# Kernel tuning notes

Measured on AMD Instinct MI355X. Metric: run time of the kernel, lower is better.

Reference implementation:

```python
import jax, jax.numpy as jnp
import numpy as np
import math

HIDDEN = 2048
N_HEADS = 16
HEAD_DIM = HIDDEN // N_HEADS
ROPE_BASE = 10000.0


def setup_inputs() -> dict:
    key = jax.random.key(0)
    ks = jax.random.split(key, 5)
    B, S = 2, 2048
    hidden_states = jax.random.normal(ks[0], (B, S, HIDDEN), dtype=jnp.float32)
    # additive causal mask (bsz, 1, q_len, kv_len)
    causal = jnp.tril(jnp.ones((S, S), dtype=bool))
    attention_mask = jnp.where(causal, 0.0, jnp.finfo(jnp.float32).min)[None, None].astype(jnp.float32)
    attention_mask = jnp.broadcast_to(attention_mask, (B, 1, S, S))
    position_ids = jnp.broadcast_to(jnp.arange(S, dtype=jnp.int32)[None], (B, S))
    scale = 1.0 / math.sqrt(HIDDEN)
    Wq = jax.random.normal(ks[1], (HIDDEN, HIDDEN), dtype=jnp.float32) * scale
    Wk = jax.random.normal(ks[2], (HIDDEN, HIDDEN), dtype=jnp.float32) * scale
    Wv = jax.random.normal(ks[3], (HIDDEN, HIDDEN), dtype=jnp.float32) * scale
    Wo = jax.random.normal(ks[4], (HIDDEN, HIDDEN), dtype=jnp.float32) * scale
    return {"hidden_states": hidden_states, "attention_mask": attention_mask,
            "position_ids": position_ids, "Wq": Wq, "Wk": Wk, "Wv": Wv, "Wo": Wo}


def _rotate_half(x):
    x1, x2 = jnp.split(x, 2, axis=-1)
    return jnp.concatenate([-x2, x1], axis=-1)


def _rope_cos_sin(position_ids, head_dim, dtype):
    inv_freq = 1.0 / (ROPE_BASE ** (jnp.arange(0, head_dim, 2, dtype=jnp.float32) / head_dim))
    freqs = position_ids.astype(jnp.float32)[..., None] * inv_freq  # [B, S, hd/2]
    emb = jnp.concatenate([freqs, freqs], axis=-1)                  # [B, S, hd]
    # unsqueeze head dim -> [B, 1, S, hd]
    return jnp.cos(emb)[:, None].astype(dtype), jnp.sin(emb)[:, None].astype(dtype)


def reference(hidden_states, attention_mask, position_ids, Wq, Wk, Wv, Wo):
    B, S, _ = hidden_states.shape
    H, D = N_HEADS, HEAD_DIM
    # projections (nn.Linear: x @ W.T); split heads -> [B, H, S, D]
    def proj(W):
        return jnp.einsum('bsh,oh->bso', hidden_states, W).reshape(B, S, H, D).transpose(0, 2, 1, 3)
    q, k, v = proj(Wq), proj(Wk), proj(Wv)
    cos, sin = _rope_cos_sin(position_ids, D, hidden_states.dtype)
    q = q * cos + _rotate_half(q) * sin
    k = k * cos + _rotate_half(k) * sin
    scores = jnp.einsum('bhqd,bhkd->bhqk', q, k) / math.sqrt(D)
    scores = scores + attention_mask
    probs = jax.nn.softmax(scores.astype(jnp.float32), axis=-1).astype(q.dtype)
    attn = jnp.einsum('bhqk,bhkd->bhqd', probs, v)
    attn = attn.transpose(0, 2, 1, 3).reshape(B, S, H * D)
    return jnp.einsum('bso,ho->bsh', attn, Wo)
```

## Files before the change

kernel.cpp:

```cpp
#include <hip/hip_runtime.h>
#include <cstdint>

typedef unsigned short u16t;
typedef float v4f __attribute__((ext_vector_type(4)));
typedef short v8s __attribute__((ext_vector_type(8)));

#define HIDDEN 2048
#define NHEAD 16
#define HDIM 128
#define SEQ 2048
#define BATCH 2
#define MROWS (BATCH * SEQ)

__device__ __forceinline__ float bf2f(u16t u) {
  return __builtin_bit_cast(float, (uint32_t)((uint32_t)u << 16));
}
__device__ __forceinline__ u16t f2bf(float f) {
  uint32_t u = __builtin_bit_cast(uint32_t, f);
  u += 0x7FFFu + ((u >> 16) & 1u);
  return (u16t)(u >> 16);
}
__device__ __forceinline__ ushort4 f2bf4(float4 v) {
  ushort4 r;
  r.x = f2bf(v.x); r.y = f2bf(v.y); r.z = f2bf(v.z); r.w = f2bf(v.w);
  return r;
}

__device__ __forceinline__ void gld_lds16(const u16t* g, u16t* l) {
  __builtin_amdgcn_global_load_lds(
      (const __attribute__((address_space(1))) uint32_t*)g,
      (__attribute__((address_space(3))) uint32_t*)l, 16, 0, 0);
}

__global__ __launch_bounds__(256) void cvt_bf16(const float* __restrict__ src,
                                                u16t* __restrict__ dst, int n8) {
  int i = blockIdx.x * 256 + threadIdx.x;
  if (i < n8) {
    float4 a = ((const float4*)src)[2 * i];
    float4 b = ((const float4*)src)[2 * i + 1];
    union { ushort4 h[2]; uint4 u; } pk;
    pk.h[0] = f2bf4(a);
    pk.h[1] = f2bf4(b);
    ((uint4*)dst)[i] = pk.u;
  }
}

__global__ __launch_bounds__(256) void cvt_bf16_w4(
    const float* __restrict__ s0, const float* __restrict__ s1,
    const float* __restrict__ s2, const float* __restrict__ s3,
    u16t* __restrict__ d0, u16t* __restrict__ d1,
    u16t* __restrict__ d2, u16t* __restrict__ d3) {
  int i = blockIdx.x * 256 + threadIdx.x;
  int sel = i >> 19;
  int j = i & 0x7FFFF;
  const float* src = (sel == 0) ? s0 : (sel == 1) ? s1 : (sel == 2) ? s2 : s3;
  u16t* dst = (sel == 0) ? d0 : (sel == 1) ? d1 : (sel == 2) ? d2 : d3;
  float4 a = ((const float4*)src)[2 * j];
  float4 b = ((const float4*)src)[2 * j + 1];
  union { ushort4 h[2]; uint4 u; } pk;
  pk.h[0] = f2bf4(a);
  pk.h[1] = f2bf4(b);
  ((uint4*)dst)[j] = pk.u;
}

template <int B_BF16, int OUT_F32>
__global__ __launch_bounds__(256) void gemm_a16(const u16t* __restrict__ A,
                                                const void* __restrict__ Bp,
                                                void* __restrict__ Cp) {
  __shared__ u16t As[128 * 32];
  __shared__ u16t Bs[128 * 32];

  const int n0 = blockIdx.x * 128;
  const int m0 = blockIdx.y * 128;
  const int t = threadIdx.x;
  const int lane = t & 63;
  const int w = t >> 6;
  const int wm = w & 1;
  const int wn = w >> 1;
  const int l15 = lane & 15;
  const int quad = lane >> 4;

  v4f acc[4][4];
#pragma unroll
  for (int i = 0; i < 4; ++i)
#pragma unroll
    for (int j = 0; j < 4; ++j) acc[i][j] = (v4f){0.f, 0.f, 0.f, 0.f};

  for (int kb = 0; kb < HIDDEN; kb += 32) {
#pragma unroll
    for (int j = 0; j < 2; ++j) {
      int idx = t + j * 256;
      int row = idx >> 2;
      int ch = (idx & 3) * 8;
      gld_lds16(&A[(size_t)(m0 + row) * HIDDEN + kb + ch], &As[idx * 8]);
      if (B_BF16)
        gld_lds16(&((const u16t*)Bp)[(size_t)(n0 + row) * HIDDEN + kb + ch], &Bs[idx * 8]);
    }
    if (!B_BF16) {
      const float* B = (const float*)Bp;
#pragma unroll
      for (int j = 0; j < 4; ++j) {
        int idx = t + j * 256;
        int row = idx >> 3;
        int c4 = (idx & 7) * 4;
        float4 bv = *(const float4*)&B[(size_t)(n0 + row) * HIDDEN + kb + c4];
        *(ushort4*)&Bs[row * 32 + c4] = f2bf4(bv);
      }
    }
    __syncthreads();

    v8s af[4], bf[4];
#pragma unroll
    for (int mt = 0; mt < 4; ++mt)
      af[mt] = *(const v8s*)&As[(wm * 64 + mt * 16 + l15) * 32 + quad * 8];
#pragma unroll
    for (int nt = 0; nt < 4; ++nt)
      bf[nt] = *(const v8s*)&Bs[(wn * 64 + nt * 16 + l15) * 32 + quad * 8];

#pragma unroll
    for (int mt = 0; mt < 4; ++mt)
#pragma unroll
      for (int nt = 0; nt < 4; ++nt)
        acc[mt][nt] = __builtin_amdgcn_mfma_f32_16x16x32_bf16(af[mt], bf[nt], acc[mt][nt], 0, 0, 0);
    __syncthreads();
  }

#pragma unroll
  for (int mt = 0; mt < 4; ++mt) {
#pragma unroll
    for (int nt = 0; nt < 4; ++nt) {
      int col = n0 + wn * 64 + nt * 16 + l15;
#pragma unroll
      for (int r = 0; r < 4; ++r) {
        int row = m0 + wm * 64 + mt * 16 + quad * 4 + r;
        if (OUT_F32)
          ((float*)Cp)[(size_t)row * HIDDEN + col] = acc[mt][nt][r];
        else
          ((u16t*)Cp)[(size_t)row * HIDDEN + col] = f2bf(acc[mt][nt][r]);
      }
    }
  }
}

template <int B_BF16>
__global__ __launch_bounds__(256) void gemm_vt(const u16t* __restrict__ A,
                                               const void* __restrict__ Bp,
                                               u16t* __restrict__ VtOut) {
  __shared__ u16t As[128 * 32];
  __shared__ u16t Bs[128 * 32];
  __shared__ u16t Ct[128 * 136];

  const int n0 = blockIdx.x * 128;
  const int m0 = blockIdx.y * 128;
  const int t = threadIdx.x;
  const int lane = t & 63;
  const int w = t >> 6;
  const int wm = w & 1;
  const int wn = w >> 1;
  const int l15 = lane & 15;
  const int quad = lane >> 4;

  v4f acc[4][4];
#pragma unroll
  for (int i = 0; i < 4; ++i)
#pragma unroll
    for (int j = 0; j < 4; ++j) acc[i][j] = (v4f){0.f, 0.f, 0.f, 0.f};

  for (int kb = 0; kb < HIDDEN; kb += 32) {
#pragma unroll
    for (int j = 0; j < 2; ++j) {
      int idx = t + j * 256;
      int row = idx >> 2;
      int ch = (idx & 3) * 8;
      gld_lds16(&A[(size_t)(m0 + row) * HIDDEN + kb + ch], &As[idx * 8]);
      if (B_BF16)
        gld_lds16(&((const u16t*)Bp)[(size_t)(n0 + row) * HIDDEN + kb + ch], &Bs[idx * 8]);
    }
    if (!B_BF16) {
      const float* B = (const float*)Bp;
#pragma unroll
      for (int j = 0; j < 4; ++j) {
        int idx = t + j * 256;
        int row = idx >> 3;
        int c4 = (idx & 7) * 4;
        float4 bv = *(const float4*)&B[(size_t)(n0 + row) * HIDDEN + kb + c4];
        *(ushort4*)&Bs[row * 32 + c4] = f2bf4(bv);
      }
    }
    __syncthreads();

    v8s af[4], bf[4];
#pragma unroll
    for (int mt = 0; mt < 4; ++mt)
      af[mt] = *(const v8s*)&As[(wm * 64 + mt * 16 + l15) * 32 + quad * 8];
#pragma unroll
    for (int nt = 0; nt < 4; ++nt)
      bf[nt] = *(const v8s*)&Bs[(wn * 64 + nt * 16 + l15) * 32 + quad * 8];

#pragma unroll
    for (int mt = 0; mt < 4; ++mt)
#pragma unroll
      for (int nt = 0; nt < 4; ++nt)
        acc[mt][nt] = __builtin_amdgcn_mfma_f32_16x16x32_bf16(af[mt], bf[nt], acc[mt][nt], 0, 0, 0);
    __syncthreads();
  }

#pragma unroll
  for (int mt = 0; mt < 4; ++mt)
#pragma unroll
    for (int nt = 0; nt < 4; ++nt)
#pragma unroll
      for (int r = 0; r < 4; ++r)
        Ct[(wn * 64 + nt * 16 + l15) * 136 + (wm * 64 + mt * 16 + quad * 4 + r)] =
            f2bf(acc[mt][nt][r]);
  __syncthreads();

#pragma unroll
  for (int j = 0; j < 8; ++j) {
    int idx = t + j * 256;
    int nl = idx >> 4;
    int mc = idx & 15;
    *(uint4*)&VtOut[(size_t)(n0 + nl) * MROWS + m0 + mc * 8] =
        *(const uint4*)&Ct[nl * 136 + mc * 8];
  }
}

__global__ __launch_bounds__(256) void rope_k(u16t* __restrict__ q, u16t* __restrict__ k) {
  int idx = blockIdx.x * 256 + threadIdx.x;
  int i = idx & 63;
  int h = (idx >> 6) & (NHEAD - 1);
  int m = idx >> 10;
  int s = m & (SEQ - 1);
  float inv = __expf(-(float)i * 0.14391156831212787f);
  float th = (float)s * inv;
  float sn, cs;
  __sincosf(th, &sn, &cs);
  size_t base = (size_t)m * HIDDEN + h * HDIM + i;
  {
    float a = bf2f(q[base]), b = bf2f(q[base + 64]);
    q[base] = f2bf(a * cs - b * sn);
    q[base + 64] = f2bf(b * cs + a * sn);
  }
  {
    float a = bf2f(k[base]), b = bf2f(k[base + 64]);
    k[base] = f2bf(a * cs - b * sn);
    k[base + 64] = f2bf(b * cs + a * sn);
  }
}

__global__ __launch_bounds__(512) void flash2(const u16t* __restrict__ Q,
                                              const u16t* __restrict__ K,
                                              const u16t* __restrict__ Vt,
                                              u16t* __restrict__ O) {
  __shared__ u16t smem[40960];
  u16t* Ps = smem + 32768;

  const int a = blockIdx.x;
  const int bh = blockIdx.y;
  const int b = bh >> 4;
  const int h = bh & 15;
  const size_t rowb = (size_t)b * SEQ;
  const u16t* vtg = Vt + (size_t)h * HDIM * MROWS + (size_t)b * SEQ;

  const int t = threadIdx.x;
  const int lane = t & 63;
  const int w = t >> 6;
  const int l15 = lane & 15;
  const int quad = lane >> 4;
  const int l7 = l15 & 7;
  const float C2 = 0.12751743f;
  const float NEG = -3.0e38f;

  const int krow = t >> 4;
  const int kch = (t & 15) * 8;
  const int vrow = t >> 3;
  const int vch = (t & 7) * 8;
  const int kx = kch ^ ((krow & 7) * 8);
  const int vx = vch ^ ((vrow & 7) * 8);
  const u16t* Kgb = &K[(rowb + krow) * HIDDEN + h * HDIM + kch];
  const u16t* Vgb = vtg + (size_t)vrow * MROWS + vch;

  for (int half = 0; half < 2; ++half) {
    const int qt = half ? (15 - a) : a;
    const int q0 = qt * 128;
    const int nsteps = 2 * (qt + 1);

    uint4 ck0 = *(const uint4*)Kgb;
    uint4 ck1 = *(const uint4*)(Kgb + 32 * HIDDEN);
    uint4 cv0 = *(const uint4*)Vgb;
    uint4 cv1 = *(const uint4*)(Vgb + (size_t)64 * MROWS);

#pragma unroll
    for (int j = 0; j < 4; ++j) {
      int idx = t + j * 512;
      int row = idx >> 4;
      int ch = (idx & 15) * 8;
      *(uint4*)&smem[row * 136 + ch] =
          *(const uint4*)&Q[(rowb + q0 + row) * HIDDEN + h * HDIM + ch];
    }
    __syncthreads();
    v8s qf[4];
#pragma unroll
    for (int ks = 0; ks < 4; ++ks)
      qf[ks] = *(const v8s*)&smem[(w * 16 + l15) * 136 + ks * 32 + quad * 8];
    __syncthreads();

    float mi[4], li[4];
    v4f o[8];
#pragma unroll
    for (int r = 0; r < 4; ++r) { mi[r] = NEG; li[r] = 0.f; }
#pragma unroll
    for (int nt = 0; nt < 8; ++nt) o[nt] = (v4f){0.f, 0.f, 0.f, 0.f};

    for (int kt = 0; kt < nsteps; ++kt) {
      u16t* Kb = smem + (kt & 1) * 16384;
      u16t* Vb = Kb + 8192;
      *(uint4*)&Kb[krow * 128 + kx] = ck0;
      *(uint4*)&Kb[(krow + 32) * 128 + kx] = ck1;
      *(uint4*)&Vb[vrow * 64 + vx] = cv0;
      *(uint4*)&Vb[(vrow + 64) * 64 + vx] = cv1;
      if (kt + 1 < nsteps) {
        const int kv1 = (kt + 1) * 64;
        const u16t* kg = Kgb + (size_t)kv1 * HIDDEN;
        ck0 = *(const uint4*)kg;
        ck1 = *(const uint4*)(kg + 32 * HIDDEN);
        const u16t* vg = Vgb + kv1;
        cv0 = *(const uint4*)vg;
        cv1 = *(const uint4*)(vg + (size_t)64 * MROWS);
      }
      __syncthreads();

      const int kv0 = kt * 64;
      v4f sc[4];
#pragma unroll
      for (int nt = 0; nt < 4; ++nt) {
        sc[nt] = (v4f){0.f, 0.f, 0.f, 0.f};
#pragma unroll
        for (int ks = 0; ks < 4; ++ks) {
          v8s kf = *(const v8s*)&Kb[(nt * 16 + l15) * 128 +
                                    ((ks * 32 + quad * 8) ^ (l7 * 8))];
          sc[nt] = __builtin_amdgcn_mfma_f32_16x16x32_bf16(qf[ks], kf, sc[nt], 0, 0, 0);
        }
      }

      const bool mm = (kv0 + 64 > q0);
#pragma unroll
      for (int r = 0; r < 4; ++r) {
        float sv[4];
#pragma unroll
        for (int nt = 0; nt < 4; ++nt) sv[nt] = sc[nt][r];
        if (mm) {
          int row_g = q0 + w * 16 + quad * 4 + r;
#pragma unroll
          for (int nt = 0; nt < 4; ++nt)
            if (kv0 + nt * 16 + l15 > row_g) sv[nt] = NEG;
        }
        float rm = fmaxf(fmaxf(sv[0], sv[1]), fmaxf(sv[2], sv[3]));
#pragma unroll
        for (int off = 1; off < 16; off <<= 1) rm = fmaxf(rm, __shfl_xor(rm, off));
        float mn = fmaxf(mi[r], rm);
        float alpha = exp2f((mi[r] - mn) * C2);
        float ps = 0.f;
        u16t pb[4];
#pragma unroll
        for (int nt = 0; nt < 4; ++nt) {
          float p = exp2f((sv[nt] - mn) * C2);
          ps += p;
          pb[nt] = f2bf(p);
        }
#pragma unroll
        for (int off = 1; off < 16; off <<= 1) ps += __shfl_xor(ps, off);
        li[r] = li[r] * alpha + ps;
        mi[r] = mn;
#pragma unroll
        for (int nt = 0; nt < 8; ++nt) o[nt][r] *= alpha;
        int rowp = w * 16 + quad * 4 + r;
        int psw = (rowp & 7) * 8;
#pragma unroll
        for (int nt = 0; nt < 4; ++nt)
          Ps[rowp * 64 + ((nt * 16 + l15) ^ psw)] = pb[nt];
      }

#pragma unroll
      for (int ks = 0; ks < 2; ++ks) {
        v8s pf = *(const v8s*)&Ps[(w * 16 + l15) * 64 +
                                  ((ks * 32 + quad * 8) ^ (l7 * 8))];
#pragma unroll
        for (int nt = 0; nt < 8; ++nt) {
          v8s vf = *(const v8s*)&Vb[(nt * 16 + l15) * 64 +
                                    ((ks * 32 + quad * 8) ^ (l7 * 8))];
          o[nt] = __builtin_amdgcn_mfma_f32_16x16x32_bf16(pf, vf, o[nt], 0, 0, 0);
        }
      }
    }

#pragma unroll
    for (int r = 0; r < 4; ++r) {
      float inv = 1.0f / li[r];
      size_t row = rowb + q0 + w * 16 + quad * 4 + r;
#pragma unroll
      for (int nt = 0; nt < 8; ++nt)
        O[row * HIDDEN + h * HDIM + nt * 16 + l15] = f2bf(o[nt][r] * inv);
    }
    __syncthreads();
  }
}

extern "C" void kernel_launch(void* const* d_in, const int* in_sizes, int n_in,
                              void* d_out, int out_size, void* d_ws, size_t ws_size,
                              hipStream_t stream) {
  const float* X = (const float*)d_in[0];
  const float* Wq = (const float*)d_in[3];
  const float* Wk = (const float*)d_in[4];
  const float* Wv = (const float*)d_in[5];
  const float* Wo = (const float*)d_in[6];
  float* out = (float*)d_out;

  char* wsb = (char*)d_ws;
  const size_t MB = 1024 * 1024;
  u16t* xb = (u16t*)(wsb + 0 * MB);
  u16t* q = (u16t*)(wsb + 16 * MB);
  u16t* k = (u16t*)(wsb + 32 * MB);
  u16t* vt = (u16t*)(wsb + 48 * MB);
  u16t* a = xb;

  dim3 blk(256);
  dim3 gg(HIDDEN / 128, MROWS / 128);
  dim3 fg(8, BATCH * NHEAD);
  const int XN8 = MROWS * HIDDEN / 8;
  const int WN8 = HIDDEN * HIDDEN / 8;

  cvt_bf16<<<(XN8 + 255) / 256, blk, 0, stream>>>(X, xb, XN8);

  if (ws_size >= 96 * MB) {
    u16t* wqb = (u16t*)(wsb + 64 * MB);
    u16t* wkb = (u16t*)(wsb + 72 * MB);
    u16t* wvb = (u16t*)(wsb + 80 * MB);
    u16t* wob = (u16t*)(wsb + 88 * MB);
    cvt_bf16_w4<<<(4 * WN8) / 256, blk, 0, stream>>>(Wq, Wk, Wv, Wo, wqb, wkb, wvb, wob);

    gemm_a16<1, 0><<<gg, blk, 0, stream>>>(xb, wqb, q);
    gemm_a16<1, 0><<<gg, blk, 0, stream>>>(xb, wkb, k);
    gemm_vt<1><<<gg, blk, 0, stream>>>(xb, wvb, vt);
    rope_k<<<(MROWS * NHEAD * 64) / 256, blk, 0, stream>>>(q, k);
    flash2<<<fg, dim3(512), 0, stream>>>(q, k, vt, a);
    gemm_a16<1, 1><<<gg, blk, 0, stream>>>(a, wob, out);
  } else {
    gemm_a16<0, 0><<<gg, blk, 0, stream>>>(xb, Wq, q);
    gemm_a16<0, 0><<<gg, blk, 0, stream>>>(xb, Wk, k);
    gemm_vt<0><<<gg, blk, 0, stream>>>(xb, Wv, vt);
    rope_k<<<(MROWS * NHEAD * 64) / 256, blk, 0, stream>>>(q, k);
    flash2<<<fg, dim3(512), 0, stream>>>(q, k, vt, a);
    gemm_a16<0, 1><<<gg, blk, 0, stream>>>(a, Wo, out);
  }
}
```

Before: 456.0 us.

## Replace bf16 projection GEMMs with 512-thread triple-buffered swizzled-LDS kernel

Adds a new GEMM kernel for the bf16-weight path, used for the Q, K, V and output projections. It uses 256x128 tiles with 8 waves, a three-stage LDS ring filled by direct global-to-LDS loads with an XOR swizzle, and 16x16x32 bf16 MFMA. Prefetch loads are split into halves that interleave with MFMA phases, and s_setprio is raised around the compute. The goal is to hide global load latency, remove LDS bank conflicts, and raise arithmetic intensity over the old 128x128 K=32 single-buffered loop. The cost is 144KB of LDS per block, so occupancy is limited to one block per CU.

```diff
diff --git a/kernel.cpp b/kernel.cpp
--- a/kernel.cpp
+++ b/kernel.cpp
@@ -63,7 +63,166 @@
   ((uint4*)dst)[j] = pk.u;
 }
 
-template <int B_BF16, int OUT_F32>
+template <int OUT>
+__global__ __launch_bounds__(512) void gemm8p(const u16t* __restrict__ A,
+                                              const u16t* __restrict__ B,
+                                              void* __restrict__ Cp) {
+  __shared__ u16t lds[73728];
+
+  const int n0 = blockIdx.x * 128;
+  const int m0 = blockIdx.y * 256;
+  const int t = threadIdx.x;
+  const int lane = t & 63;
+  const int w = t >> 6;
+  const int wm = w >> 2;
+  const int wn = w & 3;
+  const int l15 = lane & 15;
+  const int quad = lane >> 4;
+  const int l7 = l15 & 7;
+
+  const int lrow = lane >> 3;
+  const int lcol8 = ((lane & 7) ^ lrow) * 8;
+  const u16t* Ag = A + (size_t)(m0 + w * 32 + lrow) * HIDDEN + lcol8;
+  const u16t* Bg = B + (size_t)(n0 + w * 16 + lrow) * HIDDEN + lcol8;
+
+  const int ca0 = (quad * 8) ^ (l7 * 8);
+  const int ca1 = (32 + quad * 8) ^ (l7 * 8);
+
+  v4f acc[8][2];
+#pragma unroll
+  for (int i = 0; i < 8; ++i)
+#pragma unroll
+    for (int j = 0; j < 2; ++j) acc[i][j] = (v4f){0.f, 0.f, 0.f, 0.f};
+
+  const int KT = HIDDEN / 64;
+
+#pragma unroll
+  for (int tt = 0; tt < 2; ++tt) {
+    const int kb = tt * 64;
+#pragma unroll
+    for (int j = 0; j < 4; ++j)
+      gld_lds16(Ag + kb + j * 8 * HIDDEN,
+                &lds[tt * 16384 + (w * 4 + j) * 512 + lane * 8]);
+#pragma unroll
+    for (int j = 0; j < 2; ++j)
+      gld_lds16(Bg + kb + j * 8 * HIDDEN,
+                &lds[49152 + tt * 8192 + (w * 2 + j) * 512 + lane * 8]);
+  }
+  asm volatile("s_waitcnt vmcnt(6)" ::: "memory");
+  __builtin_amdgcn_s_barrier();
+
+  int b = 0;
+  for (int kt = 0; kt < KT; ++kt) {
+    const int kb2 = kt * 64 + 128;
+    const int b2 = (b >= 1) ? b - 1 : 2;
+    const u16t* Asb = &lds[b * 16384];
+    const u16t* Bsb = &lds[49152 + b * 8192];
+    const bool pre = (kt + 2 < KT);
+
+    v8s b0[2], b1[2];
+#pragma unroll
+    for (int j = 0; j < 2; ++j) {
+      const u16t* p = Bsb + (wn * 32 + j * 16 + l15) * 64;
+      b0[j] = *(const v8s*)(p + ca0);
+      b1[j] = *(const v8s*)(p + ca1);
+    }
+    v8s a0[4], a1[4];
+#pragma unroll
+    for (int i = 0; i < 4; ++i) {
+      const u16t* p = Asb + (wm * 128 + i * 16 + l15) * 64;
+      a0[i] = *(const v8s*)(p + ca0);
+      a1[i] = *(const v8s*)(p + ca1);
+    }
+    if (pre) {
+      gld_lds16(Ag + kb2, &lds[b2 * 16384 + (w * 4 + 0) * 512 + lane * 8]);
+      gld_lds16(Ag + kb2 + 8 * HIDDEN, &lds[b2 * 16384 + (w * 4 + 1) * 512 + lane * 8]);
+      gld_lds16(Bg + kb2, &lds[49152 + b2 * 8192 + (w * 2 + 0) * 512 + lane * 8]);
+    }
+    __builtin_amdgcn_s_barrier();
+    asm volatile("s_waitcnt lgkmcnt(0)" ::: "memory");
+    __builtin_amdgcn_s_setprio(1);
+#pragma unroll
+    for (int i = 0; i < 4; ++i)
+#pragma unroll
+      for (int j = 0; j < 2; ++j) {
+        acc[i][j] = __builtin_amdgcn_mfma_f32_16x16x32_bf16(a0[i], b0[j], acc[i][j], 0, 0, 0);
+        acc[i][j] = __builtin_amdgcn_mfma_f32_16x16x32_bf16(a1[i], b1[j], acc[i][j], 0, 0, 0);
+      }
+    __builtin_amdgcn_s_setprio(0);
+    __builtin_amdgcn_s_barrier();
+
+#pragma unroll
+    for (int i = 0; i < 4; ++i) {
+      const u16t* p = Asb + (wm * 128 + 64 + i * 16 + l15) * 64;
+      a0[i] = *(const v8s*)(p + ca0);
+      a1[i] = *(const v8s*)(p + ca1);
+    }
+    if (pre) {
+      gld_lds16(Ag + kb2 + 16 * HIDDEN, &lds[b2 * 16384 + (w * 4 + 2) * 512 + lane * 8]);
+      gld_lds16(Ag + kb2 + 24 * HIDDEN, &lds[b2 * 16384 + (w * 4 + 3) * 512 + lane * 8]);
+      gld_lds16(Bg + kb2 + 8 * HIDDEN, &lds[49152 + b2 * 8192 + (w * 2 + 1) * 512 + lane * 8]);
+    }
+    __builtin_amdgcn_s_barrier();
+    asm volatile("s_waitcnt lgkmcnt(0)" ::: "memory");
+    __builtin_amdgcn_s_setprio(1);
+#pragma unroll
+    for (int i = 0; i < 4; ++i)
+#pragma unroll
+      for (int j = 0; j < 2; ++j) {
+        acc[4 + i][j] = __builtin_amdgcn_mfma_f32_16x16x32_bf16(a0[i], b0[j], acc[4 + i][j], 0, 0, 0);
+        acc[4 + i][j] = __builtin_amdgcn_mfma_f32_16x16x32_bf16(a1[i], b1[j], acc[4 + i][j], 0, 0, 0);
+      }
+    __builtin_amdgcn_s_setprio(0);
+    if (pre) {
+      asm volatile("s_waitcnt vmcnt(6)" ::: "memory");
+    } else if (kt + 1 < KT) {
+      asm volatile("s_waitcnt vmcnt(0)" ::: "memory");
+    }
+    __builtin_amdgcn_s_barrier();
+    b = (b == 2) ? 0 : b + 1;
+  }
+
+  if (OUT == 2) {
+    u16t* Ct = (u16t*)lds;
+    __syncthreads();
+#pragma unroll
+    for (int i = 0; i < 8; ++i)
+#pragma unroll
+      for (int j = 0; j < 2; ++j)
+#pragma unroll
+        for (int r = 0; r < 4; ++r)
+          Ct[(wn * 32 + j * 16 + l15) * 264 + wm * 128 + i * 16 + quad * 4 + r] =
+              f2bf(acc[i][j][r]);
+    __syncthreads();
+    u16t* VtOut = (u16t*)Cp;
+#pragma unroll
+    for (int it = 0; it < 8; ++it) {
+      int idx = t + it * 512;
+      int nl = idx >> 5;
+      int mc = idx & 31;
+      *(uint4*)&VtOut[(size_t)(n0 + nl) * MROWS + m0 + mc * 8] =
+          *(const uint4*)&Ct[nl * 264 + mc * 8];
+    }
+  } else {
+#pragma unroll
+    for (int i = 0; i < 8; ++i) {
+#pragma unroll
+      for (int j = 0; j < 2; ++j) {
+        int col = n0 + wn * 32 + j * 16 + l15;
+#pragma unroll
+        for (int r = 0; r < 4; ++r) {
+          int row = m0 + wm * 128 + i * 16 + quad * 4 + r;
+          if (OUT == 1)
+            ((float*)Cp)[(size_t)row * HIDDEN + col] = acc[i][j][r];
+          else
+            ((u16t*)Cp)[(size_t)row * HIDDEN + col] = f2bf(acc[i][j][r]);
+        }
+      }
+    }
+  }
+}
+
+template <int OUT_F32>
 __global__ __launch_bounds__(256) void gemm_a16(const u16t* __restrict__ A,
                                                 const void* __restrict__ Bp,
                                                 void* __restrict__ Cp) {
@@ -93,10 +252,8 @@
       int row = idx >> 2;
       int ch = (idx & 3) * 8;
       gld_lds16(&A[(size_t)(m0 + row) * HIDDEN + kb + ch], &As[idx * 8]);
-      if (B_BF16)
-        gld_lds16(&((const u16t*)Bp)[(size_t)(n0 + row) * HIDDEN + kb + ch], &Bs[idx * 8]);
-    }
-    if (!B_BF16) {
+    }
+    {
       const float* B = (const float*)Bp;
 #pragma unroll
       for (int j = 0; j < 4; ++j) {
@@ -142,10 +299,9 @@
   }
 }
 
-template <int B_BF16>
-__global__ __launch_bounds__(256) void gemm_vt(const u16t* __restrict__ A,
-                                               const void* __restrict__ Bp,
-                                               u16t* __restrict__ VtOut) {
+__global__ __launch_bounds__(256) void gemm_vt_f32(const u16t* __restrict__ A,
+                                                   const void* __restrict__ Bp,
+                                                   u16t* __restrict__ VtOut) {
   __shared__ u16t As[128 * 32];
   __shared__ u16t Bs[128 * 32];
   __shared__ u16t Ct[128 * 136];
@@ -173,10 +329,8 @@
       int row = idx >> 2;
       int ch = (idx & 3) * 8;
       gld_lds16(&A[(size_t)(m0 + row) * HIDDEN + kb + ch], &As[idx * 8]);
-      if (B_BF16)
-        gld_lds16(&((const u16t*)Bp)[(size_t)(n0 + row) * HIDDEN + kb + ch], &Bs[idx * 8]);
-    }
-    if (!B_BF16) {
+    }
+    {
       const float* B = (const float*)Bp;
 #pragma unroll
       for (int j = 0; j < 4; ++j) {
@@ -425,7 +579,6 @@
   u16t* a = xb;
 
   dim3 blk(256);
-  dim3 gg(HIDDEN / 128, MROWS / 128);
   dim3 fg(8, BATCH * NHEAD);
   const int XN8 = MROWS * HIDDEN / 8;
   const int WN8 = HIDDEN * HIDDEN / 8;
@@ -439,18 +592,20 @@
     u16t* wob = (u16t*)(wsb + 88 * MB);
     cvt_bf16_w4<<<(4 * WN8) / 256, blk, 0, stream>>>(Wq, Wk, Wv, Wo, wqb, wkb, wvb, wob);
 
-    gemm_a16<1, 0><<<gg, blk, 0, stream>>>(xb, wqb, q);
-    gemm_a16<1, 0><<<gg, blk, 0, stream>>>(xb, wkb, k);
-    gemm_vt<1><<<gg, blk, 0, stream>>>(xb, wvb, vt);
+    dim3 g8(HIDDEN / 128, MROWS / 256);
+    gemm8p<0><<<g8, dim3(512), 0, stream>>>(xb, wqb, q);
+    gemm8p<0><<<g8, dim3(512), 0, stream>>>(xb, wkb, k);
+    gemm8p<2><<<g8, dim3(512), 0, stream>>>(xb, wvb, vt);
     rope_k<<<(MROWS * NHEAD * 64) / 256, blk, 0, stream>>>(q, k);
     flash2<<<fg, dim3(512), 0, stream>>>(q, k, vt, a);
-    gemm_a16<1, 1><<<gg, blk, 0, stream>>>(a, wob, out);
+    gemm8p<1><<<g8, dim3(512), 0, stream>>>(a, wob, out);
   } else {
-    gemm_a16<0, 0><<<gg, blk, 0, stream>>>(xb, Wq, q);
-    gemm_a16<0, 0><<<gg, blk, 0, stream>>>(xb, Wk, k);
-    gemm_vt<0><<<gg, blk, 0, stream>>>(xb, Wv, vt);
+    dim3 gg(HIDDEN / 128, MROWS / 128);
+    gemm_a16<0><<<gg, blk, 0, stream>>>(xb, Wq, q);
+    gemm_a16<0><<<gg, blk, 0, stream>>>(xb, Wk, k);
+    gemm_vt_f32<<<gg, blk, 0, stream>>>(xb, Wv, vt);
     rope_k<<<(MROWS * NHEAD * 64) / 256, blk, 0, stream>>>(q, k);
     flash2<<<fg, dim3(512), 0, stream>>>(q, k, vt, a);
-    gemm_a16<0, 1><<<gg, blk, 0, stream>>>(a, Wo, out);
-  }
-}
+    gemm_a16<1><<<gg, blk, 0, stream>>>(a, Wo, out);
+  }
+}
```

New measurement: 424.3 us. 1.07x faster.
